# Optimization experiments

Measured on AMD Instinct MI355X. Metric: run time of the kernel, lower is better.

Reference implementation:

```python
import jax, jax.numpy as jnp
import numpy as np

EPS = 1e-5

def setup_inputs() -> dict:
    key = jax.random.key(0)
    ks = jax.random.split(key, 4)
    B, C, H, W = 16, 256, 64, 64
    x = jax.random.normal(ks[0], (B, C, H, W), dtype=jnp.float32)
    w_qkv = jax.random.normal(ks[1], (3 * C, C), dtype=jnp.float32) * (C ** -0.5)
    w_proj = jax.random.normal(ks[2], (C, C), dtype=jnp.float32) * (C ** -0.5)
    b_proj = jnp.zeros((C,), dtype=jnp.float32)
    gamma = jnp.ones((C,), dtype=jnp.float32)
    beta = jnp.zeros((C,), dtype=jnp.float32)
    return {"x": x, "w_qkv": w_qkv, "w_proj": w_proj, "b_proj": b_proj,
            "gamma": gamma, "beta": beta}

def reference(x, w_qkv, w_proj, b_proj, gamma, beta):
    B, C, H, W = x.shape
    num_heads = 8
    head_dim = C // num_heads
    scale = head_dim ** -0.5
    # LayerNorm over channels (applied in BHWC layout)
    xc = x.transpose(0, 2, 3, 1)                       # (B,H,W,C)
    mu = xc.mean(axis=-1, keepdims=True)
    var = ((xc - mu) ** 2).mean(axis=-1, keepdims=True)
    xn = (xc - mu) * jax.lax.rsqrt(var + EPS) * gamma + beta
    # 1x1 conv qkv: (B,H,W,C) x (3C,C) -> (B,H,W,3C)
    qkv = jnp.einsum('bhwc,dc->bhwd', xn, w_qkv)
    qkv = qkv.reshape(B, H, W, 3, num_heads, head_dim)
    q, k, v = qkv[..., 0, :, :], qkv[..., 1, :, :], qkv[..., 2, :, :]  # (B,H,W,nh,hd)
    # attention along the W axis, independently per (batch, head, row H)
    attn = jnp.einsum('bhqnd,bhknd->bhnqk', q, k) * scale   # (B,H,nh,W,W)
    attn = jax.nn.softmax(attn, axis=-1)
    out = jnp.einsum('bhnqk,bhknd->bhqnd', attn, v)          # (B,H,W,nh,hd)
    out = out.reshape(B, H, W, C)
    # 1x1 conv proj
    out = jnp.einsum('bhwc,dc->bhwd', out, w_proj) + b_proj
    return out.transpose(0, 3, 1, 2)                         # (B,C,H,W)
```

## Files before the change

kernel.cpp:

```cpp
#include <hip/hip_runtime.h>

typedef _Float16 f16;
typedef _Float16 f16x8 __attribute__((ext_vector_type(8)));
typedef float f32x4 __attribute__((ext_vector_type(4)));

#define XNS 264
#define QKS 40
#define VTS 72
#define PSS 72

__device__ __forceinline__ f32x4 mfma16(f16x8 a, f16x8 b, f32x4 c){
  return __builtin_amdgcn_mfma_f32_16x16x32_f16(a, b, c, 0, 0, 0);
}

__global__ __launch_bounds__(256) void k_cvt(const float* __restrict__ wqkv,
                                             const float* __restrict__ wproj,
                                             f16* __restrict__ wqkv_h,
                                             f16* __restrict__ wproj_h){
  int i = blockIdx.x*256 + threadIdx.x;
  for (int idx = i; idx < 768*256; idx += gridDim.x*256) wqkv_h[idx] = (f16)wqkv[idx];
  for (int idx = i; idx < 256*256; idx += gridDim.x*256) wproj_h[idx] = (f16)wproj[idx];
}

__global__ __launch_bounds__(512, 2) void k_fused(const float* __restrict__ x,
    const float* __restrict__ gamma, const float* __restrict__ beta,
    const f16* __restrict__ wqkv, const f16* __restrict__ wproj,
    const float* __restrict__ bproj, float* __restrict__ out)
{
  __shared__ __align__(16) f16 xn[64*XNS];
  __shared__ __align__(16) f16 perw[8][7424];
  __shared__ float red[2][8][64];
  __shared__ float mrs2[2][64];

  const int t = threadIdx.x;
  const int lane = t & 63;
  const int h = t >> 6;
  const int l15 = lane & 15, l16 = lane >> 4;
  const int row = blockIdx.x;
  const int b = row >> 6, hh = row & 63;
  const float* xrow = x + (size_t)b*256*4096 + hh*64;

  f16x8 bq[16];
  {
    const f16* wq = wqkv + (size_t)(h*32)*256;
    #pragma unroll
    for (int n = 0; n < 2; ++n)
      #pragma unroll
      for (int kk = 0; kk < 8; ++kk)
        bq[n*8+kk] = *(const f16x8*)&wq[(size_t)(n*16 + l15)*256 + kk*32 + l16*8];
  }

  {
    float4 xv[8];
    #pragma unroll
    for (int it = 0; it < 8; ++it){
      int c = it*32 + h*4 + l16;
      xv[it] = *(const float4*)&xrow[(size_t)c*4096 + l15*4];
    }
    #pragma unroll
    for (int it = 0; it < 8; ++it){
      int c = it*32 + h*4 + l16;
      int w0 = l15*4;
      xn[(w0+0)*XNS + c] = (f16)xv[it].x;
      xn[(w0+1)*XNS + c] = (f16)xv[it].y;
      xn[(w0+2)*XNS + c] = (f16)xv[it].z;
      xn[(w0+3)*XNS + c] = (f16)xv[it].w;
    }
  }
  __syncthreads();

  {
    float ssum = 0.f, s2 = 0.f;
    #pragma unroll
    for (int j8 = 0; j8 < 4; ++j8){
      f16x8 v = *(const f16x8*)&xn[lane*XNS + h*32 + j8*8];
      #pragma unroll
      for (int e = 0; e < 8; ++e){ float f = (float)v[e]; ssum += f; s2 += f*f; }
    }
    red[0][h][lane] = ssum; red[1][h][lane] = s2;
  }
  __syncthreads();
  if (t < 64){
    float ss = 0.f, qq = 0.f;
    for (int j = 0; j < 8; ++j){ ss += red[0][j][t]; qq += red[1][j][t]; }
    float mu = ss*(1.f/256.f);
    float var = qq*(1.f/256.f) - mu*mu;
    mrs2[0][t] = mu; mrs2[1][t] = rsqrtf(var + 1e-5f);
  }
  __syncthreads();
  {
    float mu = mrs2[0][lane], rs = mrs2[1][lane];
    #pragma unroll
    for (int j8 = 0; j8 < 4; ++j8){
      f16x8 v = *(const f16x8*)&xn[lane*XNS + h*32 + j8*8];
      f16x8 o;
      #pragma unroll
      for (int e = 0; e < 8; ++e){
        int c = h*32 + j8*8 + e;
        o[e] = (f16)(((float)v[e] - mu)*rs*gamma[c] + beta[c]);
      }
      *(f16x8*)&xn[lane*XNS + h*32 + j8*8] = o;
    }
  }
  __syncthreads();

  f16* qs  = &perw[h][0];
  f16* ks  = &perw[h][2560];
  f16* vts = &perw[h][5120];
  f16* ps  = &perw[h][0];

  f16x8 bk[16];
  {
    const f16* wk = wqkv + (size_t)(256 + h*32)*256;
    #pragma unroll
    for (int n = 0; n < 2; ++n)
      #pragma unroll
      for (int kk = 0; kk < 8; ++kk)
        bk[n*8+kk] = *(const f16x8*)&wk[(size_t)(n*16 + l15)*256 + kk*32 + l16*8];
  }
  {
    f32x4 acc[4][2] = {};
    #pragma unroll
    for (int kk = 0; kk < 8; ++kk){
      int k0 = kk*32 + l16*8;
      f16x8 a[4];
      #pragma unroll
      for (int m = 0; m < 4; ++m) a[m] = *(const f16x8*)&xn[(m*16 + l15)*XNS + k0];
      #pragma unroll
      for (int m = 0; m < 4; ++m)
        #pragma unroll
        for (int n = 0; n < 2; ++n)
          acc[m][n] = mfma16(a[m], bq[n*8+kk], acc[m][n]);
    }
    #pragma unroll
    for (int m = 0; m < 4; ++m)
      for (int n = 0; n < 2; ++n)
        for (int r = 0; r < 4; ++r)
          qs[(m*16 + l16*4 + r)*QKS + n*16 + l15] = (f16)acc[m][n][r];
  }

  f16x8 bv[16];
  {
    const f16* wv = wqkv + (size_t)(512 + h*32)*256;
    #pragma unroll
    for (int n = 0; n < 2; ++n)
      #pragma unroll
      for (int kk = 0; kk < 8; ++kk)
        bv[n*8+kk] = *(const f16x8*)&wv[(size_t)(n*16 + l15)*256 + kk*32 + l16*8];
  }
  {
    f32x4 acc[4][2] = {};
    #pragma unroll
    for (int kk = 0; kk < 8; ++kk){
      int k0 = kk*32 + l16*8;
      f16x8 a[4];
      #pragma unroll
      for (int m = 0; m < 4; ++m) a[m] = *(const f16x8*)&xn[(m*16 + l15)*XNS + k0];
      #pragma unroll
      for (int m = 0; m < 4; ++m)
        #pragma unroll
        for (int n = 0; n < 2; ++n)
          acc[m][n] = mfma16(a[m], bk[n*8+kk], acc[m][n]);
    }
    #pragma unroll
    for (int m = 0; m < 4; ++m)
      for (int n = 0; n < 2; ++n)
        for (int r = 0; r < 4; ++r)
          ks[(m*16 + l16*4 + r)*QKS + n*16 + l15] = (f16)acc[m][n][r];
  }

  {
    f32x4 acc[2][4] = {};
    #pragma unroll
    for (int kk = 0; kk < 8; ++kk){
      int k0 = kk*32 + l16*8;
      f16x8 bb[4];
      #pragma unroll
      for (int n = 0; n < 4; ++n) bb[n] = *(const f16x8*)&xn[(n*16 + l15)*XNS + k0];
      #pragma unroll
      for (int m = 0; m < 2; ++m)
        #pragma unroll
        for (int n = 0; n < 4; ++n)
          acc[m][n] = mfma16(bv[m*8+kk], bb[n], acc[m][n]);
    }
    #pragma unroll
    for (int m = 0; m < 2; ++m)
      for (int n = 0; n < 4; ++n)
        for (int r = 0; r < 4; ++r){
          int d   = m*16 + l16*4 + r;
          int pos = n*16 + l15;
          vts[d*VTS + pos] = (f16)acc[m][n][r];
        }
  }

  f16x8 bp[16];
  {
    const f16* wp = wproj + (size_t)(h*32)*256;
    #pragma unroll
    for (int n = 0; n < 2; ++n)
      #pragma unroll
      for (int kk = 0; kk < 8; ++kk)
        bp[n*8+kk] = *(const f16x8*)&wp[(size_t)(n*16 + l15)*256 + kk*32 + l16*8];
  }
  __syncthreads();

  f32x4 sa[4][4];
  {
    int k0 = l16*8;
    f16x8 a[4], bb[4];
    #pragma unroll
    for (int m = 0; m < 4; ++m) a[m]  = *(const f16x8*)&qs[(m*16 + l15)*QKS + k0];
    #pragma unroll
    for (int n = 0; n < 4; ++n) bb[n] = *(const f16x8*)&ks[(n*16 + l15)*QKS + k0];
    f32x4 z = {0.f,0.f,0.f,0.f};
    #pragma unroll
    for (int m = 0; m < 4; ++m)
      #pragma unroll
      for (int n = 0; n < 4; ++n)
        sa[m][n] = mfma16(a[m], bb[n], z);
  }
  {
    const float sc = 0.17677669529663687f;
    #pragma unroll
    for (int m = 0; m < 4; ++m)
      #pragma unroll
      for (int r = 0; r < 4; ++r){
        float mx = fmaxf(fmaxf(sa[m][0][r], sa[m][1][r]), fmaxf(sa[m][2][r], sa[m][3][r]));
        mx = fmaxf(mx, __shfl_xor(mx, 1));
        mx = fmaxf(mx, __shfl_xor(mx, 2));
        mx = fmaxf(mx, __shfl_xor(mx, 4));
        mx = fmaxf(mx, __shfl_xor(mx, 8));
        float pv[4], sum = 0.f;
        #pragma unroll
        for (int n = 0; n < 4; ++n){ float p = __expf((sa[m][n][r] - mx)*sc); pv[n] = p; sum += p; }
        sum += __shfl_xor(sum, 1);
        sum += __shfl_xor(sum, 2);
        sum += __shfl_xor(sum, 4);
        sum += __shfl_xor(sum, 8);
        float inv = 1.f/sum;
        int q = m*16 + l16*4 + r;
        #pragma unroll
        for (int n = 0; n < 4; ++n) ps[q*PSS + n*16 + l15] = (f16)(pv[n]*inv);
      }
  }
  f16* al = xn;
  {
    f32x4 oa[4][2] = {};
    #pragma unroll
    for (int kk = 0; kk < 2; ++kk){
      int k0 = kk*32 + l16*8;
      f16x8 a[4], bb[2];
      #pragma unroll
      for (int m = 0; m < 4; ++m) a[m]  = *(const f16x8*)&ps[(m*16 + l15)*PSS + k0];
      #pragma unroll
      for (int n = 0; n < 2; ++n) bb[n] = *(const f16x8*)&vts[(n*16 + l15)*VTS + k0];
      #pragma unroll
      for (int m = 0; m < 4; ++m)
        #pragma unroll
        for (int n = 0; n < 2; ++n)
          oa[m][n] = mfma16(a[m], bb[n], oa[m][n]);
    }
    #pragma unroll
    for (int m = 0; m < 4; ++m)
      for (int n = 0; n < 2; ++n)
        for (int r = 0; r < 4; ++r){
          int pos = m*16 + l16*4 + r;
          al[pos*XNS + h*32 + n*16 + l15] = (f16)oa[m][n][r];
        }
  }
  __syncthreads();

  {
    f32x4 acc[4][2] = {};
    #pragma unroll
    for (int kk = 0; kk < 8; ++kk){
      int k0 = kk*32 + l16*8;
      f16x8 a[4];
      #pragma unroll
      for (int m = 0; m < 4; ++m) a[m] = *(const f16x8*)&al[(m*16 + l15)*XNS + k0];
      #pragma unroll
      for (int m = 0; m < 4; ++m)
        #pragma unroll
        for (int n = 0; n < 2; ++n)
          acc[m][n] = mfma16(a[m], bp[n*8+kk], acc[m][n]);
    }
    float bia[2];
    #pragma unroll
    for (int n = 0; n < 2; ++n) bia[n] = bproj[h*32 + n*16 + l15];
    float* obase = out + (size_t)b*256*4096 + hh*64;
    #pragma unroll
    for (int m = 0; m < 4; ++m)
      #pragma unroll
      for (int n = 0; n < 2; ++n){
        int dout = h*32 + n*16 + l15;
        f32x4 v;
        #pragma unroll
        for (int r = 0; r < 4; ++r) v[r] = acc[m][n][r] + bia[n];
        *(f32x4*)&obase[(size_t)dout*4096 + m*16 + l16*4] = v;
      }
  }
}

extern "C" void kernel_launch(void* const* d_in, const int* in_sizes, int n_in,
                              void* d_out, int out_size, void* d_ws, size_t ws_size,
                              hipStream_t stream)
{
  const float* x     = (const float*)d_in[0];
  const float* wqkv  = (const float*)d_in[1];
  const float* wproj = (const float*)d_in[2];
  const float* bproj = (const float*)d_in[3];
  const float* gamma = (const float*)d_in[4];
  const float* beta  = (const float*)d_in[5];
  float* out = (float*)d_out;

  f16* ws = (f16*)d_ws;
  f16* wqkv_h  = ws;
  f16* wproj_h = ws + 196608;

  k_cvt  <<<256, 256, 0, stream>>>(wqkv, wproj, wqkv_h, wproj_h);
  k_fused<<<1024, 512, 0, stream>>>(x, gamma, beta, wqkv_h, wproj_h, bproj, out);
}
```

Before: 211.4 us.

## Halve block to four waves, each processing two attention heads sequentially

Result: faster. 201.7 us (-4.6%).

```diff
diff --git a/kernel.cpp b/kernel.cpp
--- a/kernel.cpp
+++ b/kernel.cpp
@@ -1,13 +1,15 @@
 #include <hip/hip_runtime.h>
 
 typedef _Float16 f16;
+typedef _Float16 f16x4 __attribute__((ext_vector_type(4)));
 typedef _Float16 f16x8 __attribute__((ext_vector_type(8)));
 typedef float f32x4 __attribute__((ext_vector_type(4)));
 
 #define XNS 264
 #define QKS 40
 #define VTS 72
-#define PSS 72
+#define PSS 40
+#define SLOT 5120
 
 __device__ __forceinline__ f32x4 mfma16(f16x8 a, f16x8 b, f32x4 c){
   return __builtin_amdgcn_mfma_f32_16x16x32_f16(a, b, c, 0, 0, 0);
@@ -22,277 +24,303 @@
   for (int idx = i; idx < 256*256; idx += gridDim.x*256) wproj_h[idx] = (f16)wproj[idx];
 }
 
-__global__ __launch_bounds__(512, 2) void k_fused(const float* __restrict__ x,
+__global__ __launch_bounds__(256, 2) void k_fused(const float* __restrict__ x,
     const float* __restrict__ gamma, const float* __restrict__ beta,
     const f16* __restrict__ wqkv, const f16* __restrict__ wproj,
     const float* __restrict__ bproj, float* __restrict__ out)
 {
   __shared__ __align__(16) f16 xn[64*XNS];
-  __shared__ __align__(16) f16 perw[8][7424];
-  __shared__ float red[2][8][64];
-  __shared__ float mrs2[2][64];
+  __shared__ __align__(16) f16 perw[4][SLOT];
 
   const int t = threadIdx.x;
   const int lane = t & 63;
-  const int h = t >> 6;
+  const int w = t >> 6;
   const int l15 = lane & 15, l16 = lane >> 4;
   const int row = blockIdx.x;
   const int b = row >> 6, hh = row & 63;
   const float* xrow = x + (size_t)b*256*4096 + hh*64;
 
-  f16x8 bq[16];
-  {
-    const f16* wq = wqkv + (size_t)(h*32)*256;
+  f16x8 bq[2][16];
+  {
+    const f16* wq = wqkv + (size_t)(w*32)*256;
     #pragma unroll
     for (int n = 0; n < 2; ++n)
       #pragma unroll
       for (int kk = 0; kk < 8; ++kk)
-        bq[n*8+kk] = *(const f16x8*)&wq[(size_t)(n*16 + l15)*256 + kk*32 + l16*8];
-  }
-
-  {
-    float4 xv[8];
-    #pragma unroll
-    for (int it = 0; it < 8; ++it){
-      int c = it*32 + h*4 + l16;
-      xv[it] = *(const float4*)&xrow[(size_t)c*4096 + l15*4];
-    }
-    #pragma unroll
-    for (int it = 0; it < 8; ++it){
-      int c = it*32 + h*4 + l16;
-      int w0 = l15*4;
-      xn[(w0+0)*XNS + c] = (f16)xv[it].x;
-      xn[(w0+1)*XNS + c] = (f16)xv[it].y;
-      xn[(w0+2)*XNS + c] = (f16)xv[it].z;
-      xn[(w0+3)*XNS + c] = (f16)xv[it].w;
+        bq[0][n*8+kk] = *(const f16x8*)&wq[(size_t)(n*16 + l15)*256 + kk*32 + l16*8];
+  }
+
+  {
+    const int c = t;
+    #pragma unroll
+    for (int j = 0; j < 16; ++j){
+      float4 v = *(const float4*)&xrow[(size_t)c*4096 + j*4];
+      xn[(j*4+0)*XNS + c] = (f16)v.x;
+      xn[(j*4+1)*XNS + c] = (f16)v.y;
+      xn[(j*4+2)*XNS + c] = (f16)v.z;
+      xn[(j*4+3)*XNS + c] = (f16)v.w;
     }
   }
   __syncthreads();
 
-  {
-    float ssum = 0.f, s2 = 0.f;
-    #pragma unroll
-    for (int j8 = 0; j8 < 4; ++j8){
-      f16x8 v = *(const f16x8*)&xn[lane*XNS + h*32 + j8*8];
-      #pragma unroll
-      for (int e = 0; e < 8; ++e){ float f = (float)v[e]; ssum += f; s2 += f*f; }
-    }
-    red[0][h][lane] = ssum; red[1][h][lane] = s2;
+  float mu, rs;
+  {
+    float* red = (float*)&perw[0][0];
+    float s = 0.f, s2 = 0.f;
+    #pragma unroll
+    for (int j8 = 0; j8 < 8; ++j8){
+      f16x8 v = *(const f16x8*)&xn[lane*XNS + w*64 + j8*8];
+      #pragma unroll
+      for (int e = 0; e < 8; ++e){ float f = (float)v[e]; s += f; s2 += f*f; }
+    }
+    red[w*64 + lane] = s;
+    red[256 + w*64 + lane] = s2;
+    __syncthreads();
+    float ss = 0.f, qq = 0.f;
+    #pragma unroll
+    for (int j = 0; j < 4; ++j){ ss += red[j*64 + lane]; qq += red[256 + j*64 + lane]; }
+    mu = ss*(1.f/256.f);
+    rs = rsqrtf(qq*(1.f/256.f) - mu*mu + 1e-5f);
+  }
+  {
+    #pragma unroll
+    for (int j8 = 0; j8 < 8; ++j8){
+      int c0 = w*64 + j8*8;
+      f16x8 v = *(const f16x8*)&xn[lane*XNS + c0];
+      f16x8 o;
+      #pragma unroll
+      for (int e = 0; e < 8; ++e)
+        o[e] = (f16)(((float)v[e] - mu)*rs*gamma[c0+e] + beta[c0+e]);
+      *(f16x8*)&xn[lane*XNS + c0] = o;
+    }
   }
   __syncthreads();
-  if (t < 64){
-    float ss = 0.f, qq = 0.f;
-    for (int j = 0; j < 8; ++j){ ss += red[0][j][t]; qq += red[1][j][t]; }
-    float mu = ss*(1.f/256.f);
-    float var = qq*(1.f/256.f) - mu*mu;
-    mrs2[0][t] = mu; mrs2[1][t] = rsqrtf(var + 1e-5f);
+
+  f16* qs  = &perw[w][0];
+  f16* ks  = &perw[w][2560];
+  f16* vts = &perw[w][2560];
+  f16* ps  = &perw[w][0];
+
+  f16x4 oh[2][4][2];
+  f16x8 bk[16], bv[16], bplo[16];
+
+  #pragma unroll
+  for (int hi = 0; hi < 2; ++hi){
+    const int head = w + hi*4;
+
+    {
+      const f16* wk = wqkv + (size_t)(256 + head*32)*256;
+      #pragma unroll
+      for (int n = 0; n < 2; ++n)
+        #pragma unroll
+        for (int kk = 0; kk < 8; ++kk)
+          bk[n*8+kk] = *(const f16x8*)&wk[(size_t)(n*16 + l15)*256 + kk*32 + l16*8];
+    }
+    {
+      f32x4 acc[4][2] = {};
+      #pragma unroll
+      for (int kk = 0; kk < 8; ++kk){
+        int k0 = kk*32 + l16*8;
+        f16x8 a[4];
+        #pragma unroll
+        for (int m = 0; m < 4; ++m) a[m] = *(const f16x8*)&xn[(m*16 + l15)*XNS + k0];
+        #pragma unroll
+        for (int m = 0; m < 4; ++m)
+          #pragma unroll
+          for (int n = 0; n < 2; ++n)
+            acc[m][n] = mfma16(a[m], bq[hi][n*8+kk], acc[m][n]);
+      }
+      #pragma unroll
+      for (int m = 0; m < 4; ++m)
+        for (int n = 0; n < 2; ++n)
+          for (int r = 0; r < 4; ++r)
+            qs[(m*16 + l16*4 + r)*QKS + n*16 + l15] = (f16)acc[m][n][r];
+    }
+    {
+      const f16* wv = wqkv + (size_t)(512 + head*32)*256;
+      #pragma unroll
+      for (int n = 0; n < 2; ++n)
+        #pragma unroll
+        for (int kk = 0; kk < 8; ++kk)
+          bv[n*8+kk] = *(const f16x8*)&wv[(size_t)(n*16 + l15)*256 + kk*32 + l16*8];
+    }
+    {
+      f32x4 acc[4][2] = {};
+      #pragma unroll
+      for (int kk = 0; kk < 8; ++kk){
+        int k0 = kk*32 + l16*8;
+        f16x8 a[4];
+        #pragma unroll
+        for (int m = 0; m < 4; ++m) a[m] = *(const f16x8*)&xn[(m*16 + l15)*XNS + k0];
+        #pragma unroll
+        for (int m = 0; m < 4; ++m)
+          #pragma unroll
+          for (int n = 0; n < 2; ++n)
+            acc[m][n] = mfma16(a[m], bk[n*8+kk], acc[m][n]);
+      }
+      #pragma unroll
+      for (int m = 0; m < 4; ++m)
+        for (int n = 0; n < 2; ++n)
+          for (int r = 0; r < 4; ++r)
+            ks[(m*16 + l16*4 + r)*QKS + n*16 + l15] = (f16)acc[m][n][r];
+    }
+    f32x4 sa[4][4];
+    {
+      int k0 = l16*8;
+      f16x8 a[4], bb[4];
+      #pragma unroll
+      for (int m = 0; m < 4; ++m) a[m]  = *(const f16x8*)&qs[(m*16 + l15)*QKS + k0];
+      #pragma unroll
+      for (int n = 0; n < 4; ++n) bb[n] = *(const f16x8*)&ks[(n*16 + l15)*QKS + k0];
+      f32x4 z = {0.f,0.f,0.f,0.f};
+      #pragma unroll
+      for (int m = 0; m < 4; ++m)
+        #pragma unroll
+        for (int n = 0; n < 4; ++n)
+          sa[m][n] = mfma16(a[m], bb[n], z);
+    }
+    {
+      const float sc = 0.17677669529663687f;
+      #pragma unroll
+      for (int m = 0; m < 4; ++m)
+        #pragma unroll
+        for (int r = 0; r < 4; ++r){
+          float mx = fmaxf(fmaxf(sa[m][0][r], sa[m][1][r]), fmaxf(sa[m][2][r], sa[m][3][r]));
+          mx = fmaxf(mx, __shfl_xor(mx, 1));
+          mx = fmaxf(mx, __shfl_xor(mx, 2));
+          mx = fmaxf(mx, __shfl_xor(mx, 4));
+          mx = fmaxf(mx, __shfl_xor(mx, 8));
+          float pv[4], sum = 0.f;
+          #pragma unroll
+          for (int n = 0; n < 4; ++n){ float p = __expf((sa[m][n][r] - mx)*sc); pv[n] = p; sum += p; }
+          sum += __shfl_xor(sum, 1);
+          sum += __shfl_xor(sum, 2);
+          sum += __shfl_xor(sum, 4);
+          sum += __shfl_xor(sum, 8);
+          float inv = 1.f/sum;
+          #pragma unroll
+          for (int n = 0; n < 4; ++n) sa[m][n][r] = pv[n]*inv;
+        }
+    }
+    if (hi == 0){
+      const f16* wq = wqkv + (size_t)((w+4)*32)*256;
+      #pragma unroll
+      for (int n = 0; n < 2; ++n)
+        #pragma unroll
+        for (int kk = 0; kk < 8; ++kk)
+          bq[1][n*8+kk] = *(const f16x8*)&wq[(size_t)(n*16 + l15)*256 + kk*32 + l16*8];
+    } else {
+      const f16* wp = wproj + (size_t)(w*64)*256;
+      #pragma unroll
+      for (int n = 0; n < 2; ++n)
+        #pragma unroll
+        for (int kk = 0; kk < 8; ++kk)
+          bplo[n*8+kk] = *(const f16x8*)&wp[(size_t)(n*16 + l15)*256 + kk*32 + l16*8];
+    }
+    {
+      f32x4 acc[2][4] = {};
+      #pragma unroll
+      for (int kk = 0; kk < 8; ++kk){
+        int k0 = kk*32 + l16*8;
+        f16x8 bb[4];
+        #pragma unroll
+        for (int n = 0; n < 4; ++n) bb[n] = *(const f16x8*)&xn[(n*16 + l15)*XNS + k0];
+        #pragma unroll
+        for (int m = 0; m < 2; ++m)
+          #pragma unroll
+          for (int n = 0; n < 4; ++n)
+            acc[m][n] = mfma16(bv[m*8+kk], bb[n], acc[m][n]);
+      }
+      #pragma unroll
+      for (int m = 0; m < 2; ++m)
+        for (int n = 0; n < 4; ++n)
+          for (int r = 0; r < 4; ++r){
+            int d   = m*16 + l16*4 + r;
+            int pos = n*16 + l15;
+            vts[d*VTS + pos] = (f16)acc[m][n][r];
+          }
+    }
+    {
+      f32x4 oa[4][2] = {};
+      #pragma unroll
+      for (int half = 0; half < 2; ++half){
+        #pragma unroll
+        for (int m = 0; m < 4; ++m)
+          #pragma unroll
+          for (int n2 = 0; n2 < 2; ++n2)
+            #pragma unroll
+            for (int r = 0; r < 4; ++r)
+              ps[(m*16 + l16*4 + r)*PSS + n2*16 + l15] = (f16)sa[m][half*2+n2][r];
+        int k0 = half*32 + l16*8;
+        f16x8 a[4], bb[2];
+        #pragma unroll
+        for (int m = 0; m < 4; ++m) a[m]  = *(const f16x8*)&ps[(m*16 + l15)*PSS + l16*8];
+        #pragma unroll
+        for (int n = 0; n < 2; ++n) bb[n] = *(const f16x8*)&vts[(n*16 + l15)*VTS + k0];
+        #pragma unroll
+        for (int m = 0; m < 4; ++m)
+          #pragma unroll
+          for (int n = 0; n < 2; ++n)
+            oa[m][n] = mfma16(a[m], bb[n], oa[m][n]);
+      }
+      #pragma unroll
+      for (int m = 0; m < 4; ++m)
+        #pragma unroll
+        for (int n = 0; n < 2; ++n)
+          #pragma unroll
+          for (int r = 0; r < 4; ++r)
+            oh[hi][m][n][r] = (f16)oa[m][n][r];
+    }
   }
   __syncthreads();
-  {
-    float mu = mrs2[0][lane], rs = mrs2[1][lane];
-    #pragma unroll
-    for (int j8 = 0; j8 < 4; ++j8){
-      f16x8 v = *(const f16x8*)&xn[lane*XNS + h*32 + j8*8];
-      f16x8 o;
-      #pragma unroll
-      for (int e = 0; e < 8; ++e){
-        int c = h*32 + j8*8 + e;
-        o[e] = (f16)(((float)v[e] - mu)*rs*gamma[c] + beta[c]);
-      }
-      *(f16x8*)&xn[lane*XNS + h*32 + j8*8] = o;
-    }
+
+  f16* al = &perw[0][0];
+  #pragma unroll
+  for (int hi = 0; hi < 2; ++hi){
+    int hc = (w + hi*4)*32;
+    #pragma unroll
+    for (int m = 0; m < 4; ++m)
+      for (int n = 0; n < 2; ++n)
+        for (int r = 0; r < 4; ++r)
+          al[(m*16 + l16*4 + r)*XNS + hc + n*16 + l15] = oh[hi][m][n][r];
   }
   __syncthreads();
 
-  f16* qs  = &perw[h][0];
-  f16* ks  = &perw[h][2560];
-  f16* vts = &perw[h][5120];
-  f16* ps  = &perw[h][0];
-
-  f16x8 bk[16];
-  {
-    const f16* wk = wqkv + (size_t)(256 + h*32)*256;
+  f16x8 bphi[16];
+  {
+    const f16* wp = wproj + (size_t)(w*64)*256;
     #pragma unroll
     for (int n = 0; n < 2; ++n)
       #pragma unroll
       for (int kk = 0; kk < 8; ++kk)
-        bk[n*8+kk] = *(const f16x8*)&wk[(size_t)(n*16 + l15)*256 + kk*32 + l16*8];
-  }
-  {
-    f32x4 acc[4][2] = {};
+        bphi[n*8+kk] = *(const f16x8*)&wp[(size_t)((n+2)*16 + l15)*256 + kk*32 + l16*8];
+  }
+  {
+    f32x4 acc[4][4] = {};
     #pragma unroll
     for (int kk = 0; kk < 8; ++kk){
       int k0 = kk*32 + l16*8;
       f16x8 a[4];
       #pragma unroll
-      for (int m = 0; m < 4; ++m) a[m] = *(const f16x8*)&xn[(m*16 + l15)*XNS + k0];
-      #pragma unroll
-      for (int m = 0; m < 4; ++m)
-        #pragma unroll
-        for (int n = 0; n < 2; ++n)
-          acc[m][n] = mfma16(a[m], bq[n*8+kk], acc[m][n]);
-    }
+      for (int m = 0; m < 4; ++m) a[m] = *(const f16x8*)&al[(m*16 + l15)*XNS + k0];
+      #pragma unroll
+      for (int m = 0; m < 4; ++m){
+        #pragma unroll
+        for (int n = 0; n < 2; ++n){
+          acc[m][n]   = mfma16(a[m], bplo[n*8+kk], acc[m][n]);
+          acc[m][2+n] = mfma16(a[m], bphi[n*8+kk], acc[m][2+n]);
+        }
+      }
+    }
+    float bia[4];
+    #pragma unroll
+    for (int n = 0; n < 4; ++n) bia[n] = bproj[w*64 + n*16 + l15];
+    float* obase = out + (size_t)b*256*4096 + hh*64;
     #pragma unroll
     for (int m = 0; m < 4; ++m)
-      for (int n = 0; n < 2; ++n)
-        for (int r = 0; r < 4; ++r)
-          qs[(m*16 + l16*4 + r)*QKS + n*16 + l15] = (f16)acc[m][n][r];
-  }
-
-  f16x8 bv[16];
-  {
-    const f16* wv = wqkv + (size_t)(512 + h*32)*256;
-    #pragma unroll
-    for (int n = 0; n < 2; ++n)
-      #pragma unroll
-      for (int kk = 0; kk < 8; ++kk)
-        bv[n*8+kk] = *(const f16x8*)&wv[(size_t)(n*16 + l15)*256 + kk*32 + l16*8];
-  }
-  {
-    f32x4 acc[4][2] = {};
-    #pragma unroll
-    for (int kk = 0; kk < 8; ++kk){
-      int k0 = kk*32 + l16*8;
-      f16x8 a[4];
-      #pragma unroll
-      for (int m = 0; m < 4; ++m) a[m] = *(const f16x8*)&xn[(m*16 + l15)*XNS + k0];
-      #pragma unroll
-      for (int m = 0; m < 4; ++m)
-        #pragma unroll
-        for (int n = 0; n < 2; ++n)
-          acc[m][n] = mfma16(a[m], bk[n*8+kk], acc[m][n]);
-    }
-    #pragma unroll
-    for (int m = 0; m < 4; ++m)
-      for (int n = 0; n < 2; ++n)
-        for (int r = 0; r < 4; ++r)
-          ks[(m*16 + l16*4 + r)*QKS + n*16 + l15] = (f16)acc[m][n][r];
-  }
-
-  {
-    f32x4 acc[2][4] = {};
-    #pragma unroll
-    for (int kk = 0; kk < 8; ++kk){
-      int k0 = kk*32 + l16*8;
-      f16x8 bb[4];
-      #pragma unroll
-      for (int n = 0; n < 4; ++n) bb[n] = *(const f16x8*)&xn[(n*16 + l15)*XNS + k0];
-      #pragma unroll
-      for (int m = 0; m < 2; ++m)
-        #pragma unroll
-        for (int n = 0; n < 4; ++n)
-          acc[m][n] = mfma16(bv[m*8+kk], bb[n], acc[m][n]);
-    }
-    #pragma unroll
-    for (int m = 0; m < 2; ++m)
-      for (int n = 0; n < 4; ++n)
-        for (int r = 0; r < 4; ++r){
-          int d   = m*16 + l16*4 + r;
-          int pos = n*16 + l15;
-          vts[d*VTS + pos] = (f16)acc[m][n][r];
-        }
-  }
-
-  f16x8 bp[16];
-  {
-    const f16* wp = wproj + (size_t)(h*32)*256;
-    #pragma unroll
-    for (int n = 0; n < 2; ++n)
-      #pragma unroll
-      for (int kk = 0; kk < 8; ++kk)
-        bp[n*8+kk] = *(const f16x8*)&wp[(size_t)(n*16 + l15)*256 + kk*32 + l16*8];
-  }
-  __syncthreads();
-
-  f32x4 sa[4][4];
-  {
-    int k0 = l16*8;
-    f16x8 a[4], bb[4];
-    #pragma unroll
-    for (int m = 0; m < 4; ++m) a[m]  = *(const f16x8*)&qs[(m*16 + l15)*QKS + k0];
-    #pragma unroll
-    for (int n = 0; n < 4; ++n) bb[n] = *(const f16x8*)&ks[(n*16 + l15)*QKS + k0];
-    f32x4 z = {0.f,0.f,0.f,0.f};
-    #pragma unroll
-    for (int m = 0; m < 4; ++m)
-      #pragma unroll
-      for (int n = 0; n < 4; ++n)
-        sa[m][n] = mfma16(a[m], bb[n], z);
-  }
-  {
-    const float sc = 0.17677669529663687f;
-    #pragma unroll
-    for (int m = 0; m < 4; ++m)
-      #pragma unroll
-      for (int r = 0; r < 4; ++r){
-        float mx = fmaxf(fmaxf(sa[m][0][r], sa[m][1][r]), fmaxf(sa[m][2][r], sa[m][3][r]));
-        mx = fmaxf(mx, __shfl_xor(mx, 1));
-        mx = fmaxf(mx, __shfl_xor(mx, 2));
-        mx = fmaxf(mx, __shfl_xor(mx, 4));
-        mx = fmaxf(mx, __shfl_xor(mx, 8));
-        float pv[4], sum = 0.f;
-        #pragma unroll
-        for (int n = 0; n < 4; ++n){ float p = __expf((sa[m][n][r] - mx)*sc); pv[n] = p; sum += p; }
-        sum += __shfl_xor(sum, 1);
-        sum += __shfl_xor(sum, 2);
-        sum += __shfl_xor(sum, 4);
-        sum += __shfl_xor(sum, 8);
-        float inv = 1.f/sum;
-        int q = m*16 + l16*4 + r;
-        #pragma unroll
-        for (int n = 0; n < 4; ++n) ps[q*PSS + n*16 + l15] = (f16)(pv[n]*inv);
-      }
-  }
-  f16* al = xn;
-  {
-    f32x4 oa[4][2] = {};
-    #pragma unroll
-    for (int kk = 0; kk < 2; ++kk){
-      int k0 = kk*32 + l16*8;
-      f16x8 a[4], bb[2];
-      #pragma unroll
-      for (int m = 0; m < 4; ++m) a[m]  = *(const f16x8*)&ps[(m*16 + l15)*PSS + k0];
-      #pragma unroll
-      for (int n = 0; n < 2; ++n) bb[n] = *(const f16x8*)&vts[(n*16 + l15)*VTS + k0];
-      #pragma unroll
-      for (int m = 0; m < 4; ++m)
-        #pragma unroll
-        for (int n = 0; n < 2; ++n)
-          oa[m][n] = mfma16(a[m], bb[n], oa[m][n]);
-    }
-    #pragma unroll
-    for (int m = 0; m < 4; ++m)
-      for (int n = 0; n < 2; ++n)
-        for (int r = 0; r < 4; ++r){
-          int pos = m*16 + l16*4 + r;
-          al[pos*XNS + h*32 + n*16 + l15] = (f16)oa[m][n][r];
-        }
-  }
-  __syncthreads();
-
-  {
-    f32x4 acc[4][2] = {};
-    #pragma unroll
-    for (int kk = 0; kk < 8; ++kk){
-      int k0 = kk*32 + l16*8;
-      f16x8 a[4];
-      #pragma unroll
-      for (int m = 0; m < 4; ++m) a[m] = *(const f16x8*)&al[(m*16 + l15)*XNS + k0];
-      #pragma unroll
-      for (int m = 0; m < 4; ++m)
-        #pragma unroll
-        for (int n = 0; n < 2; ++n)
-          acc[m][n] = mfma16(a[m], bp[n*8+kk], acc[m][n]);
-    }
-    float bia[2];
-    #pragma unroll
-    for (int n = 0; n < 2; ++n) bia[n] = bproj[h*32 + n*16 + l15];
-    float* obase = out + (size_t)b*256*4096 + hh*64;
-    #pragma unroll
-    for (int m = 0; m < 4; ++m)
-      #pragma unroll
-      for (int n = 0; n < 2; ++n){
-        int dout = h*32 + n*16 + l15;
+      #pragma unroll
+      for (int n = 0; n < 4; ++n){
+        int dout = w*64 + n*16 + l15;
         f32x4 v;
         #pragma unroll
         for (int r = 0; r < 4; ++r) v[r] = acc[m][n][r] + bia[n];
@@ -318,5 +346,5 @@
   f16* wproj_h = ws + 196608;
 
   k_cvt  <<<256, 256, 0, stream>>>(wqkv, wproj, wqkv_h, wproj_h);
-  k_fused<<<1024, 512, 0, stream>>>(x, gamma, beta, wqkv_h, wproj_h, bproj, out);
+  k_fused<<<1024, 256, 0, stream>>>(x, gamma, beta, wqkv_h, wproj_h, bproj, out);
 }
```
